# Optimization experiments

Measured on AMD Instinct MI355X. Metric: run time of the kernel, lower is better.

Reference implementation:

```python
import jax, jax.numpy as jnp
import numpy as np

B = 131072
IN = 128
H = 128

def setup_inputs() -> dict:
    key = jax.random.key(0)
    ks = jax.random.split(key, 12)
    # kaiming-normal-ish init for weights (std ~ sqrt(2/fan_out))
    std_w = (2.0 / H) ** 0.5
    inp = {
        'x': jax.random.normal(ks[0], (B, IN), dtype=jnp.float32),
        'h_prev': jax.random.normal(ks[1], (B, H), dtype=jnp.float32),
        'c_prev': jax.random.normal(ks[2], (B, H), dtype=jnp.float32),
        'Wi': jax.random.normal(ks[3], (IN, H), dtype=jnp.float32) * std_w,
        'Ui': jax.random.normal(ks[4], (H, H), dtype=jnp.float32) * std_w,
        'bi': jnp.ones((H,), dtype=jnp.float32),
        'Wf': jax.random.normal(ks[5], (IN, H), dtype=jnp.float32) * std_w,
        'Uf': jax.random.normal(ks[6], (H, H), dtype=jnp.float32) * std_w,
        'bf': jnp.ones((H,), dtype=jnp.float32),
        'Wg': jax.random.normal(ks[7], (IN, H), dtype=jnp.float32) * std_w,
        'Ug': jax.random.normal(ks[8], (H, H), dtype=jnp.float32) * std_w,
        'bg': jnp.ones((H,), dtype=jnp.float32),
        'Wo': jax.random.normal(ks[9], (IN, H), dtype=jnp.float32) * std_w,
        'Uo': jax.random.normal(ks[10], (H, H), dtype=jnp.float32) * std_w,
        'bo': jnp.ones((H,), dtype=jnp.float32),
    }
    return inp

def reference(x, h_prev, c_prev, Wi, Ui, bi, Wf, Uf, bf, Wg, Ug, bg, Wo, Uo, bo):
    # Faithful per-gate math (i, f, o sigmoid gates; g tanh candidate)
    ig = jax.nn.sigmoid(x @ Wi + h_prev @ Ui + bi)
    fg = jax.nn.sigmoid(x @ Wf + h_prev @ Uf + bf)
    og = jax.nn.sigmoid(x @ Wo + h_prev @ Uo + bo)
    cc = jnp.tanh(x @ Wg + h_prev @ Ug + bg)
    c = fg * c_prev + ig * cc
    h = og * jnp.tanh(c)
    return (h, c)
```

## Files before the change

kernel.cpp:

```cpp
#include <hip/hip_runtime.h>


#define B_ROWS 131072
#define HDIM 128
#define KDIM 256
#define BM 64
#define LDT 132

typedef __attribute__((ext_vector_type(4))) float f32x4;
typedef __attribute__((ext_vector_type(8))) short s16x8;

__device__ inline unsigned short f2bf(float f) {
    unsigned int u = __float_as_uint(f);
    u += 0x7fffu + ((u >> 16) & 1u);
    return (unsigned short)(u >> 16);
}

__device__ inline float frcp(float x) { return __builtin_amdgcn_rcpf(x); }
__device__ inline float fsigmoid(float x) { return frcp(1.0f + __expf(-x)); }
__device__ inline float ftanh(float x) { return 1.0f - 2.0f * frcp(__expf(2.0f * x) + 1.0f); }

__global__ void prep_weights(const float* __restrict__ Wi, const float* __restrict__ Ui,
                             const float* __restrict__ Wf, const float* __restrict__ Uf,
                             const float* __restrict__ Wg, const float* __restrict__ Ug,
                             const float* __restrict__ Wo, const float* __restrict__ Uo,
                             unsigned short* __restrict__ Bp) {
    int idx = blockIdx.x * 256 + threadIdx.x;
    int e   = idx & 7;
    int q   = (idx >> 3) & 3;
    int t16 = (idx >> 5) & 15;
    int ni  = (idx >> 9) & 3;
    int kc  = (idx >> 11) & 7;
    int w   = idx >> 14;
    int j = w * 16 + t16;
    int k = kc * 32 + q * 8 + e;
    const float* Wp = ni == 0 ? Wi : ni == 1 ? Wf : ni == 2 ? Wg : Wo;
    const float* Up = ni == 0 ? Ui : ni == 1 ? Uf : ni == 2 ? Ug : Uo;
    float v = (k < 128) ? Wp[k * HDIM + j] : Up[(k - 128) * HDIM + j];
    Bp[idx] = f2bf(v);
}

__global__ __launch_bounds__(512, 4) void lstm_main(
    const float* __restrict__ x, const float* __restrict__ h_prev,
    const float* __restrict__ c_prev,
    const unsigned short* __restrict__ Bp,
    const float* __restrict__ bi, const float* __restrict__ bf_,
    const float* __restrict__ bg, const float* __restrict__ bo,
    float* __restrict__ out)
{
    __shared__ float smem[2 * BM * LDT];
    float* hbuf = smem;
    float* cbuf = smem + BM * LDT;
    unsigned short* As = (unsigned short*)smem;

    const int tid = threadIdx.x;
    const int m0 = blockIdx.x * BM;

    float4 cpv[4];
    #pragma unroll
    for (int it = 0; it < 4; ++it) {
        int f = it * 512 + tid;
        int r = f >> 5, c4 = f & 31;
        cpv[it] = *(const float4*)(c_prev + (size_t)(m0 + r) * HDIM + c4 * 4);
    }

    #pragma unroll
    for (int it = 0; it < 8; ++it) {
        int fi = it * 512 + tid;
        int r  = fi >> 6;
        int c4 = fi & 63;
        int k0 = c4 * 4;
        const float* src = (k0 < 128) ? (x + (size_t)(m0 + r) * HDIM + k0)
                                      : (h_prev + (size_t)(m0 + r) * HDIM + (k0 - 128));
        float4 v = *(const float4*)src;
        ushort4 p;
        p.x = f2bf(v.x); p.y = f2bf(v.y); p.z = f2bf(v.z); p.w = f2bf(v.w);
        int mi = r >> 4, t16r = r & 15;
        int kc = k0 >> 5, qq = (k0 >> 3) & 3, e0 = k0 & 7;
        *(ushort4*)&As[((mi * 8 + kc) * 16 + t16r) * 32 + qq * 8 + e0] = p;
    }

    #pragma unroll
    for (int it = 0; it < 4; ++it) {
        int f = it * 512 + tid;
        int r = f >> 5, c4 = f & 31;
        *(float4*)&cbuf[r * LDT + c4 * 4] = cpv[it];
    }
    __syncthreads();

    const int wave = tid >> 6;
    const int lane = tid & 63;
    const int t16 = lane & 15;
    const int q = lane >> 4;
    const int lane_off = t16 * 32 + q * 8;

    f32x4 acc[4][4];
    const f32x4 zero = {0.0f, 0.0f, 0.0f, 0.0f};
    #pragma unroll
    for (int mi = 0; mi < 4; ++mi)
        #pragma unroll
        for (int ni = 0; ni < 4; ++ni)
            acc[mi][ni] = zero;

    const unsigned short* bbase = Bp + (size_t)(wave * 8) * 2048 + lane_off;

    #pragma unroll
    for (int kc = 0; kc < 8; ++kc) {
        s16x8 a[4], b[4];
        #pragma unroll
        for (int ni = 0; ni < 4; ++ni)
            b[ni] = *(const s16x8*)(bbase + kc * 2048 + ni * 512);
        #pragma unroll
        for (int mi = 0; mi < 4; ++mi)
            a[mi] = *(const s16x8*)&As[(mi * 8 + kc) * 512 + lane_off];
        #pragma unroll
        for (int mi = 0; mi < 4; ++mi)
            #pragma unroll
            for (int ni = 0; ni < 4; ++ni)
                acc[mi][ni] = __builtin_amdgcn_mfma_f32_16x16x32_bf16(a[mi], b[ni], acc[mi][ni], 0, 0, 0);
    }
    __syncthreads();

    const int j = wave * 16 + t16;
    const float vbi = bi[j], vbf = bf_[j], vbg = bg[j], vbo = bo[j];

    #pragma unroll
    for (int mi = 0; mi < 4; ++mi) {
        #pragma unroll
        for (int r = 0; r < 4; ++r) {
            int rt = mi * 16 + q * 4 + r;
            float cp = cbuf[rt * LDT + j];
            float ig = fsigmoid(acc[mi][0][r] + vbi);
            float fg = fsigmoid(acc[mi][1][r] + vbf);
            float cc = ftanh(acc[mi][2][r] + vbg);
            float og = fsigmoid(acc[mi][3][r] + vbo);
            float c = fg * cp + ig * cc;
            float h = og * ftanh(c);
            hbuf[rt * LDT + j] = h;
            cbuf[rt * LDT + j] = c;
        }
    }
    __syncthreads();

    float* hout = out;
    float* cout = out + (size_t)B_ROWS * HDIM;
    #pragma unroll
    for (int it = 0; it < 4; ++it) {
        int f = it * 512 + tid;
        int r = f >> 5, c4 = f & 31;
        size_t goff = (size_t)(m0 + r) * HDIM + c4 * 4;
        *(float4*)(hout + goff) = *(const float4*)&hbuf[r * LDT + c4 * 4];
        *(float4*)(cout + goff) = *(const float4*)&cbuf[r * LDT + c4 * 4];
    }
}

extern "C" void kernel_launch(void* const* d_in, const int* in_sizes, int n_in,
                              void* d_out, int out_size, void* d_ws, size_t ws_size,
                              hipStream_t stream) {
    const float* x      = (const float*)d_in[0];
    const float* h_prev = (const float*)d_in[1];
    const float* c_prev = (const float*)d_in[2];
    const float* Wi = (const float*)d_in[3];
    const float* Ui = (const float*)d_in[4];
    const float* bi = (const float*)d_in[5];
    const float* Wf = (const float*)d_in[6];
    const float* Uf = (const float*)d_in[7];
    const float* bf = (const float*)d_in[8];
    const float* Wg = (const float*)d_in[9];
    const float* Ug = (const float*)d_in[10];
    const float* bg = (const float*)d_in[11];
    const float* Wo = (const float*)d_in[12];
    const float* Uo = (const float*)d_in[13];
    const float* bo = (const float*)d_in[14];

    unsigned short* Bp = (unsigned short*)d_ws;

    prep_weights<<<512, 256, 0, stream>>>(Wi, Ui, Wf, Uf, Wg, Ug, Wo, Uo, Bp);
    lstm_main<<<B_ROWS / BM, 512, 0, stream>>>(x, h_prev, c_prev, Bp, bi, bf, bg, bo, (float*)d_out);
}
```

Before: 332.4 us.

## Pre-convert x and h_prev to bf16 in a separate pass; load A fragments from global

A new kernel converts x and h_prev into a packed bf16 row-major buffer in workspace. The main kernel then reads MFMA A operands directly from global memory instead of staging them through LDS, which removes the LDS write pass and one barrier. Weight loads become nontemporal. The cost is an extra global round trip: 128 MB of fp32 reads plus 64 MB of bf16 writes, then 64 MB of bf16 rereads. The direct global A loads are also strided per lane, which may coalesce poorly.

```diff
diff --git a/kernel.cpp b/kernel.cpp
--- a/kernel.cpp
+++ b/kernel.cpp
@@ -3,7 +3,6 @@
 
 #define B_ROWS 131072
 #define HDIM 128
-#define KDIM 256
 #define BM 64
 #define LDT 132
 
@@ -40,8 +39,26 @@
     Bp[idx] = f2bf(v);
 }
 
+__global__ __launch_bounds__(256) void prep_xh(const float* __restrict__ x,
+                                               const float* __restrict__ h_prev,
+                                               unsigned short* __restrict__ XH) {
+    int idx = blockIdx.x * 256 + threadIdx.x;
+    int r  = idx >> 5;
+    int k0 = (idx & 31) * 8;
+    const float* src = (k0 < 128) ? (x + (size_t)r * HDIM + k0)
+                                  : (h_prev + (size_t)r * HDIM + (k0 - 128));
+    float4 v0 = *(const float4*)src;
+    float4 v1 = *(const float4*)(src + 4);
+    ushort4 p0, p1;
+    p0.x = f2bf(v0.x); p0.y = f2bf(v0.y); p0.z = f2bf(v0.z); p0.w = f2bf(v0.w);
+    p1.x = f2bf(v1.x); p1.y = f2bf(v1.y); p1.z = f2bf(v1.z); p1.w = f2bf(v1.w);
+    unsigned short* dst = XH + (size_t)r * 256 + k0;
+    *(ushort4*)dst = p0;
+    *(ushort4*)(dst + 4) = p1;
+}
+
 __global__ __launch_bounds__(512, 4) void lstm_main(
-    const float* __restrict__ x, const float* __restrict__ h_prev,
+    const unsigned short* __restrict__ XH,
     const float* __restrict__ c_prev,
     const unsigned short* __restrict__ Bp,
     const float* __restrict__ bi, const float* __restrict__ bf_,
@@ -51,10 +68,14 @@
     __shared__ float smem[2 * BM * LDT];
     float* hbuf = smem;
     float* cbuf = smem + BM * LDT;
-    unsigned short* As = (unsigned short*)smem;
 
     const int tid = threadIdx.x;
     const int m0 = blockIdx.x * BM;
+    const int wave = tid >> 6;
+    const int lane = tid & 63;
+    const int t16 = lane & 15;
+    const int q = lane >> 4;
+    const int lane_off = t16 * 32 + q * 8;
 
     float4 cpv[4];
     #pragma unroll
@@ -63,36 +84,15 @@
         int r = f >> 5, c4 = f & 31;
         cpv[it] = *(const float4*)(c_prev + (size_t)(m0 + r) * HDIM + c4 * 4);
     }
-
-    #pragma unroll
-    for (int it = 0; it < 8; ++it) {
-        int fi = it * 512 + tid;
-        int r  = fi >> 6;
-        int c4 = fi & 63;
-        int k0 = c4 * 4;
-        const float* src = (k0 < 128) ? (x + (size_t)(m0 + r) * HDIM + k0)
-                                      : (h_prev + (size_t)(m0 + r) * HDIM + (k0 - 128));
-        float4 v = *(const float4*)src;
-        ushort4 p;
-        p.x = f2bf(v.x); p.y = f2bf(v.y); p.z = f2bf(v.z); p.w = f2bf(v.w);
-        int mi = r >> 4, t16r = r & 15;
-        int kc = k0 >> 5, qq = (k0 >> 3) & 3, e0 = k0 & 7;
-        *(ushort4*)&As[((mi * 8 + kc) * 16 + t16r) * 32 + qq * 8 + e0] = p;
-    }
-
     #pragma unroll
     for (int it = 0; it < 4; ++it) {
         int f = it * 512 + tid;
         int r = f >> 5, c4 = f & 31;
         *(float4*)&cbuf[r * LDT + c4 * 4] = cpv[it];
     }
-    __syncthreads();
 
-    const int wave = tid >> 6;
-    const int lane = tid & 63;
-    const int t16 = lane & 15;
-    const int q = lane >> 4;
-    const int lane_off = t16 * 32 + q * 8;
+    const unsigned short* abase = XH + (size_t)(m0 + t16) * 256 + q * 8;
+    const unsigned short* bbase = Bp + (size_t)(wave * 8) * 2048 + lane_off;
 
     f32x4 acc[4][4];
     const f32x4 zero = {0.0f, 0.0f, 0.0f, 0.0f};
@@ -102,17 +102,15 @@
         for (int ni = 0; ni < 4; ++ni)
             acc[mi][ni] = zero;
 
-    const unsigned short* bbase = Bp + (size_t)(wave * 8) * 2048 + lane_off;
-
     #pragma unroll
     for (int kc = 0; kc < 8; ++kc) {
         s16x8 a[4], b[4];
         #pragma unroll
         for (int ni = 0; ni < 4; ++ni)
-            b[ni] = *(const s16x8*)(bbase + kc * 2048 + ni * 512);
+            b[ni] = __builtin_nontemporal_load((const s16x8*)(bbase + kc * 2048 + ni * 512));
         #pragma unroll
         for (int mi = 0; mi < 4; ++mi)
-            a[mi] = *(const s16x8*)&As[(mi * 8 + kc) * 512 + lane_off];
+            a[mi] = *(const s16x8*)(abase + mi * 4096 + kc * 32);
         #pragma unroll
         for (int mi = 0; mi < 4; ++mi)
             #pragma unroll
@@ -173,8 +171,10 @@
     const float* Uo = (const float*)d_in[13];
     const float* bo = (const float*)d_in[14];
 
-    unsigned short* Bp = (unsigned short*)d_ws;
+    unsigned short* XH = (unsigned short*)d_ws;
+    unsigned short* Bp = (unsigned short*)((char*)d_ws + (size_t)67108864);
 
     prep_weights<<<512, 256, 0, stream>>>(Wi, Ui, Wf, Uf, Wg, Ug, Wo, Uo, Bp);
-    lstm_main<<<B_ROWS / BM, 512, 0, stream>>>(x, h_prev, c_prev, Bp, bi, bf, bg, bo, (float*)d_out);
+    prep_xh<<<16384, 256, 0, stream>>>(x, h_prev, XH);
+    lstm_main<<<B_ROWS / BM, 512, 0, stream>>>(XH, c_prev, Bp, bi, bf, bg, bo, (float*)d_out);
 }
```

Result: slower. 455.1 us (+36.9%).
